# Kernel tuning notes

Hardware: AMD Instinct MI355X
Metric: run time of the kernel (lower is better)

The kernel has to match this reference:

```python
import jax, jax.numpy as jnp
import numpy as np

B, H, L, DK = 1, 16, 2048, 64
F_FACTOR = 64            # f
MAX_SEQ = 2048           # max_seq_len
RB = MAX_SEQ // F_FACTOR # 32, out dim of f_b


def setup_inputs() -> dict:
    key = jax.random.key(0)
    ks = jax.random.split(key, 6)
    q = jax.random.normal(ks[0], (B, H, L, DK), dtype=jnp.float32)
    v = jax.random.normal(ks[1], (B, H, L, DK), dtype=jnp.float32)
    # nn.Linear weights: [out_features, in_features]
    Wa = jax.random.normal(ks[2], (F_FACTOR, DK), dtype=jnp.float32) / np.sqrt(DK)
    ba = jax.random.normal(ks[3], (F_FACTOR,), dtype=jnp.float32) * 0.02
    Wb = jax.random.normal(ks[4], (RB, DK), dtype=jnp.float32) / np.sqrt(DK)
    bb = jax.random.normal(ks[5], (RB,), dtype=jnp.float32) * 0.02
    return {"q": q, "v": v, "Wa": Wa, "ba": ba, "Wb": Wb, "bb": bb, "len_q": L}


def reference(q, v, Wa, ba, Wb, bb, len_q):
    f = Wa.shape[0]            # f
    rb = Wb.shape[0]           # max_seq_len // f
    # h_a: repeat each of the f factor channels (max_seq_len//f) times -> [B,H,L,max_seq_len], slice to len_q
    h_a = jnp.repeat(q @ Wa.T + ba, rb, axis=-1)[..., :len_q]
    # h_b: repeat each of the (max_seq_len//f) channels f times
    h_b = jnp.repeat(q @ Wb.T + bb, f, axis=-1)[..., :len_q]
    # dense_attn = h_a @ h_b^T  -> [B,H,L,L]
    dense_attn = jnp.einsum('bhik,bhjk->bhij', h_a, h_b)
    # mask=None path; dropout inactive (eval / p=0)
    dense_attn = jax.nn.softmax(dense_attn, axis=-1)
    output = jnp.matmul(dense_attn, v)  # [B,H,L,DK]
    return (output, dense_attn)
```

## Files before the change

kernel.cpp:

```cpp
#include <hip/hip_runtime.h>
#include <hip/hip_bf16.h>


#define HN 16
#define LN 2048
#define KR 32

typedef __attribute__((ext_vector_type(8))) short bf16x8;
typedef __attribute__((ext_vector_type(4))) float f32x4;

__device__ __forceinline__ float b2f(unsigned short u) {
    return __uint_as_float(((unsigned int)u) << 16);
}
__device__ __forceinline__ unsigned short f2b(float f) {
    __hip_bfloat16 h = __float2bfloat16(f);
    return *reinterpret_cast<unsigned short*>(&h);
}

__global__ __launch_bounds__(256) void k_cb(
    const float* __restrict__ q,
    const float* __restrict__ Wa, const float* __restrict__ ba,
    const float* __restrict__ Wb, const float* __restrict__ bb,
    unsigned short* __restrict__ Chi, unsigned short* __restrict__ Clo,
    unsigned short* __restrict__ Bhi, unsigned short* __restrict__ Blo)
{
    __shared__ float sWa[64 * 64];
    __shared__ float sWb[32 * 64];
    __shared__ float sba[64];
    __shared__ float sbb[32];
    const int tid = threadIdx.x;
    for (int i = tid; i < 64 * 64; i += 256) sWa[i] = Wa[i];
    for (int i = tid; i < 32 * 64; i += 256) sWb[i] = Wb[i];
    if (tid < 64) sba[tid] = ba[tid];
    if (tid < 32) sbb[tid] = bb[tid];
    __syncthreads();

    const int t = blockIdx.x * 256 + tid;
    const int row = t >> 2, mh = (t & 3) * 8;
    float qf[64];
    const float4* q4p = reinterpret_cast<const float4*>(q + (size_t)row * 64);
    #pragma unroll
    for (int k4 = 0; k4 < 16; ++k4) {
        float4 u = q4p[k4];
        qf[4*k4+0] = u.x; qf[4*k4+1] = u.y; qf[4*k4+2] = u.z; qf[4*k4+3] = u.w;
    }
    const int ob = row * KR;
    #pragma unroll 1
    for (int mi = 0; mi < 8; ++mi) {
        const int m = mh + mi;
        float a0 = sba[2*m], a1 = sba[2*m+1], bv = sbb[m];
        const float4* wa0 = reinterpret_cast<const float4*>(&sWa[(2*m) * 64]);
        const float4* wa1 = reinterpret_cast<const float4*>(&sWa[(2*m+1) * 64]);
        const float4* wb0 = reinterpret_cast<const float4*>(&sWb[m * 64]);
        #pragma unroll
        for (int k4 = 0; k4 < 16; ++k4) {
            float4 w0 = wa0[k4], w1 = wa1[k4], w2 = wb0[k4];
            float x0 = qf[4*k4], x1 = qf[4*k4+1], x2 = qf[4*k4+2], x3 = qf[4*k4+3];
            a0 = fmaf(x0, w0.x, a0); a0 = fmaf(x1, w0.y, a0);
            a0 = fmaf(x2, w0.z, a0); a0 = fmaf(x3, w0.w, a0);
            a1 = fmaf(x0, w1.x, a1); a1 = fmaf(x1, w1.y, a1);
            a1 = fmaf(x2, w1.z, a1); a1 = fmaf(x3, w1.w, a1);
            bv = fmaf(x0, w2.x, bv); bv = fmaf(x1, w2.y, bv);
            bv = fmaf(x2, w2.z, bv); bv = fmaf(x3, w2.w, bv);
        }
        float c = 32.f * (a0 + a1);
        unsigned short ch = f2b(c);
        Chi[ob + m] = ch; Clo[ob + m] = f2b(c - b2f(ch));
        unsigned short bh = f2b(bv);
        Bhi[ob + m] = bh; Blo[ob + m] = f2b(bv - b2f(bh));
    }
}

__global__ __launch_bounds__(256) void k_vt(
    const float* __restrict__ v, unsigned short* __restrict__ Vt)
{
    __shared__ unsigned short sv[64 * 66];
    const int tid = threadIdx.x;
    const int h = blockIdx.x >> 5, jt = blockIdx.x & 31;
    const float* src = v + (size_t)(h * LN + jt * 64) * 64;
    for (int i = tid; i < 4096; i += 256)
        sv[(i >> 6) * 66 + (i & 63)] = f2b(src[i]);
    __syncthreads();
    for (int i = tid; i < 4096; i += 256) {
        int d = i >> 6, j = i & 63;
        Vt[(size_t)(h * 64 + d) * LN + jt * 64 + j] = sv[j * 66 + d];
    }
}

__global__ __launch_bounds__(256) void k_pvs(
    const unsigned short* __restrict__ Chi, const unsigned short* __restrict__ Clo,
    const unsigned short* __restrict__ Bhi, const unsigned short* __restrict__ Blo,
    const unsigned short* __restrict__ Vt,
    float* __restrict__ outO, float* __restrict__ outP)
{
    __shared__ unsigned short Ps[4][16 * 68];
    __shared__ float Psf[4][16 * 68];
    const int b = blockIdx.x;
    const int h = (b & 7) * 2 + (b >> 8);
    const int tile = (b >> 3) & 31;
    const int tid = threadIdx.x, w = tid >> 6, lane = tid & 63;
    const int quad = lane >> 4, n16 = lane & 15;
    const int rbase = tile * 64 + w * 16;
    const int hL = h * LN;
    unsigned short* ps = &Ps[w][0];
    float* psf = &Psf[w][0];

    const bf16x8 ahi = *reinterpret_cast<const bf16x8*>(Chi + (size_t)(hL + rbase + n16) * KR + quad * 8);
    const bf16x8 alo = *reinterpret_cast<const bf16x8*>(Clo + (size_t)(hL + rbase + n16) * KR + quad * 8);

    const unsigned short* bhiP = Bhi + (size_t)(hL + n16) * KR + quad * 8;
    const unsigned short* bloP = Blo + (size_t)(hL + n16) * KR + quad * 8;

    const unsigned short* vrow[4];
    #pragma unroll
    for (int di = 0; di < 4; ++di)
        vrow[di] = Vt + (size_t)(h * 64 + di * 16 + n16) * LN + quad * 8;

    f32x4 zero = {0.f, 0.f, 0.f, 0.f};

    float m0[4] = {-1e30f, -1e30f, -1e30f, -1e30f};
    float l0[4] = {0.f, 0.f, 0.f, 0.f};
    for (int jc = 0; jc < 32; ++jc) {
        const int jb = jc * 64;
        f32x4 s[4];
        #pragma unroll
        for (int ni = 0; ni < 4; ++ni) {
            const int off = (jb + ni * 16) * KR;
            bf16x8 bhi = *reinterpret_cast<const bf16x8*>(bhiP + off);
            bf16x8 blo = *reinterpret_cast<const bf16x8*>(bloP + off);
            f32x4 acc = zero;
            acc = __builtin_amdgcn_mfma_f32_16x16x32_bf16(ahi, bhi, acc, 0, 0, 0);
            acc = __builtin_amdgcn_mfma_f32_16x16x32_bf16(ahi, blo, acc, 0, 0, 0);
            acc = __builtin_amdgcn_mfma_f32_16x16x32_bf16(alo, bhi, acc, 0, 0, 0);
            acc = __builtin_amdgcn_mfma_f32_16x16x32_bf16(alo, blo, acc, 0, 0, 0);
            s[ni] = acc;
        }
        #pragma unroll
        for (int r = 0; r < 4; ++r) {
            float v0 = s[0][r], v1 = s[1][r], v2 = s[2][r], v3 = s[3][r];
            float mx = fmaxf(fmaxf(v0, v1), fmaxf(v2, v3));
            float mn = fmaxf(m0[r], mx);
            l0[r] = l0[r] * __expf(m0[r] - mn)
                  + __expf(v0 - mn) + __expf(v1 - mn)
                  + __expf(v2 - mn) + __expf(v3 - mn);
            m0[r] = mn;
        }
    }
    #pragma unroll
    for (int off = 1; off <= 8; off <<= 1) {
        #pragma unroll
        for (int r = 0; r < 4; ++r) {
            float m2 = __shfl_xor(m0[r], off, 64);
            float l2 = __shfl_xor(l0[r], off, 64);
            float mn = fmaxf(m0[r], m2);
            l0[r] = l0[r] * __expf(m0[r] - mn) + l2 * __expf(m2 - mn);
            m0[r] = mn;
        }
    }
    float mr[4], li[4];
    #pragma unroll
    for (int r = 0; r < 4; ++r) { mr[r] = m0[r]; li[r] = 1.f / l0[r]; }

    f32x4 o[4];
    #pragma unroll
    for (int di = 0; di < 4; ++di) o[di] = zero;

    for (int jc = 0; jc < 32; ++jc) {
        const int jb = jc * 64;
        #pragma unroll
        for (int ni = 0; ni < 4; ++ni) {
            const int off = (jb + ni * 16) * KR;
            bf16x8 bhi = *reinterpret_cast<const bf16x8*>(bhiP + off);
            bf16x8 blo = *reinterpret_cast<const bf16x8*>(bloP + off);
            f32x4 acc = zero;
            acc = __builtin_amdgcn_mfma_f32_16x16x32_bf16(ahi, bhi, acc, 0, 0, 0);
            acc = __builtin_amdgcn_mfma_f32_16x16x32_bf16(ahi, blo, acc, 0, 0, 0);
            acc = __builtin_amdgcn_mfma_f32_16x16x32_bf16(alo, bhi, acc, 0, 0, 0);
            acc = __builtin_amdgcn_mfma_f32_16x16x32_bf16(alo, blo, acc, 0, 0, 0);
            #pragma unroll
            for (int r = 0; r < 4; ++r) {
                float p = __expf(acc[r] - mr[r]) * li[r];
                const int sidx = (quad * 4 + r) * 68 + ni * 16 + n16;
                psf[sidx] = p;
                ps[sidx] = f2b(p);
            }
        }
        #pragma unroll
        for (int rr = 0; rr < 4; ++rr) {
            const int prow = rr * 4 + quad;
            const int pcol = n16 * 4;
            f32x4 val = *reinterpret_cast<f32x4*>(psf + prow * 68 + pcol);
            __builtin_nontemporal_store(val,
                reinterpret_cast<f32x4*>(outP + (size_t)(hL + rbase + prow) * LN + jb + pcol));
        }
        #pragma unroll
        for (int ks = 0; ks < 2; ++ks) {
            const bf16x8 pa = *reinterpret_cast<const bf16x8*>(ps + n16 * 68 + ks * 32 + quad * 8);
            #pragma unroll
            for (int di = 0; di < 4; ++di) {
                const bf16x8 vb = *reinterpret_cast<const bf16x8*>(vrow[di] + jb + ks * 32);
                o[di] = __builtin_amdgcn_mfma_f32_16x16x32_bf16(pa, vb, o[di], 0, 0, 0);
            }
        }
    }
    #pragma unroll
    for (int di = 0; di < 4; ++di) {
        #pragma unroll
        for (int r = 0; r < 4; ++r) {
            const int grow = rbase + quad * 4 + r;
            __builtin_nontemporal_store(o[di][r],
                &outO[(size_t)(hL + grow) * 64 + di * 16 + n16]);
        }
    }
}

extern "C" void kernel_launch(void* const* d_in, const int* in_sizes, int n_in,
                              void* d_out, int out_size, void* d_ws, size_t ws_size,
                              hipStream_t stream)
{
    (void)in_sizes; (void)n_in; (void)out_size; (void)ws_size;
    const float* q  = (const float*)d_in[0];
    const float* v  = (const float*)d_in[1];
    const float* Wa = (const float*)d_in[2];
    const float* ba = (const float*)d_in[3];
    const float* Wb = (const float*)d_in[4];
    const float* bb = (const float*)d_in[5];

    float* out = (float*)d_out;
    char* wsb = (char*)d_ws;
    const size_t CBb = (size_t)HN * LN * KR * 2;
    unsigned short* Chi = (unsigned short*)(wsb + 0 * CBb);
    unsigned short* Clo = (unsigned short*)(wsb + 1 * CBb);
    unsigned short* Bhi = (unsigned short*)(wsb + 2 * CBb);
    unsigned short* Blo = (unsigned short*)(wsb + 3 * CBb);
    unsigned short* Vt  = (unsigned short*)(wsb + 4 * CBb);

    float* outO = out;
    float* outP = out + (size_t)HN * LN * 64;

    hipLaunchKernelGGL(k_cb, dim3(512), dim3(256), 0, stream,
                       q, Wa, ba, Wb, bb, Chi, Clo, Bhi, Blo);
    hipLaunchKernelGGL(k_vt, dim3(512), dim3(256), 0, stream, v, Vt);
    hipLaunchKernelGGL(k_pvs, dim3(512), dim3(256), 0, stream,
                       Chi, Clo, Bhi, Blo, Vt, outO, outP);
}
```

Measured before the change: 449.6 us.

## Pack B and V into per-chunk fragment tiles staged via direct global-to-LDS loads

The B hi/lo factors and transposed V are now written into a combined per-head, per-64-column tile whose layout matches the MFMA fragment order. The attention kernel stages each tile into shared memory with global_load_lds and reads its fragments from LDS instead of issuing scattered global loads per wave. The producer kernels gain vectorized 16-byte stores. The cost is two block barriers per chunk iteration and extra LDS, with no double buffering, so load latency is no longer hidden by per-wave independence.

```diff
diff --git a/kernel.cpp b/kernel.cpp
--- a/kernel.cpp
+++ b/kernel.cpp
@@ -16,13 +16,20 @@
     __hip_bfloat16 h = __float2bfloat16(f);
     return *reinterpret_cast<unsigned short*>(&h);
 }
+__device__ __forceinline__ void glds16(const void* g, void* l) {
+    __builtin_amdgcn_global_load_lds(
+        (const __attribute__((address_space(1))) unsigned int*)g,
+        (__attribute__((address_space(3))) unsigned int*)l, 16, 0, 0);
+}
+
+#define TILE_SH 8192
 
 __global__ __launch_bounds__(256) void k_cb(
     const float* __restrict__ q,
     const float* __restrict__ Wa, const float* __restrict__ ba,
     const float* __restrict__ Wb, const float* __restrict__ bb,
     unsigned short* __restrict__ Chi, unsigned short* __restrict__ Clo,
-    unsigned short* __restrict__ Bhi, unsigned short* __restrict__ Blo)
+    unsigned short* __restrict__ Tile)
 {
     __shared__ float sWa[64 * 64];
     __shared__ float sWb[32 * 64];
@@ -36,7 +43,10 @@
     __syncthreads();
 
     const int t = blockIdx.x * 256 + tid;
-    const int row = t >> 2, mh = (t & 3) * 8;
+    const int row = t >> 2, kg = t & 3, mh = kg * 8;
+    const int h = row >> 11, i = row & 2047;
+    const int jc = i >> 6, c = i & 63;
+
     float qf[64];
     const float4* q4p = reinterpret_cast<const float4*>(q + (size_t)row * 64);
     #pragma unroll
@@ -44,8 +54,8 @@
         float4 u = q4p[k4];
         qf[4*k4+0] = u.x; qf[4*k4+1] = u.y; qf[4*k4+2] = u.z; qf[4*k4+3] = u.w;
     }
-    const int ob = row * KR;
-    #pragma unroll 1
+    unsigned short chb[8], clb[8], bhb[8], blb[8];
+    #pragma unroll
     for (int mi = 0; mi < 8; ++mi) {
         const int m = mh + mi;
         float a0 = sba[2*m], a1 = sba[2*m+1], bv = sbb[m];
@@ -63,36 +73,48 @@
             bv = fmaf(x0, w2.x, bv); bv = fmaf(x1, w2.y, bv);
             bv = fmaf(x2, w2.z, bv); bv = fmaf(x3, w2.w, bv);
         }
-        float c = 32.f * (a0 + a1);
-        unsigned short ch = f2b(c);
-        Chi[ob + m] = ch; Clo[ob + m] = f2b(c - b2f(ch));
+        float cc = 32.f * (a0 + a1);
+        unsigned short ch = f2b(cc);
+        chb[mi] = ch; clb[mi] = f2b(cc - b2f(ch));
         unsigned short bh = f2b(bv);
-        Bhi[ob + m] = bh; Blo[ob + m] = f2b(bv - b2f(bh));
-    }
-}
-
-__global__ __launch_bounds__(256) void k_vt(
-    const float* __restrict__ v, unsigned short* __restrict__ Vt)
+        bhb[mi] = bh; blb[mi] = f2b(bv - b2f(bh));
+    }
+    *reinterpret_cast<uint4*>(Chi + (size_t)row * KR + mh) = *reinterpret_cast<uint4*>(chb);
+    *reinterpret_cast<uint4*>(Clo + (size_t)row * KR + mh) = *reinterpret_cast<uint4*>(clb);
+    unsigned short* tb = Tile + (size_t)(h * 32 + jc) * TILE_SH + (kg * 64 + c) * 8;
+    *reinterpret_cast<uint4*>(tb)        = *reinterpret_cast<uint4*>(bhb);
+    *reinterpret_cast<uint4*>(tb + 2048) = *reinterpret_cast<uint4*>(blb);
+}
+
+__global__ __launch_bounds__(256) void k_vtc(
+    const float* __restrict__ v, unsigned short* __restrict__ Tile)
 {
     __shared__ unsigned short sv[64 * 66];
     const int tid = threadIdx.x;
-    const int h = blockIdx.x >> 5, jt = blockIdx.x & 31;
-    const float* src = v + (size_t)(h * LN + jt * 64) * 64;
+    const int h = blockIdx.x >> 5, jc = blockIdx.x & 31;
+    const float* src = v + (size_t)(h * LN + jc * 64) * 64;
     for (int i = tid; i < 4096; i += 256)
         sv[(i >> 6) * 66 + (i & 63)] = f2b(src[i]);
     __syncthreads();
-    for (int i = tid; i < 4096; i += 256) {
-        int d = i >> 6, j = i & 63;
-        Vt[(size_t)(h * 64 + d) * LN + jt * 64 + j] = sv[j * 66 + d];
+    unsigned short* vt = Tile + (size_t)(h * 32 + jc) * TILE_SH + 4096;
+    #pragma unroll
+    for (int it = 0; it < 2; ++it) {
+        const int gi = tid + it * 256;
+        const int jg = gi >> 6, d = gi & 63;
+        unsigned short g8[8];
+        #pragma unroll
+        for (int cjj = 0; cjj < 8; ++cjj)
+            g8[cjj] = sv[(jg * 8 + cjj) * 66 + d];
+        *reinterpret_cast<uint4*>(vt + (jg * 64 + d) * 8) = *reinterpret_cast<uint4*>(g8);
     }
 }
 
 __global__ __launch_bounds__(256) void k_pvs(
     const unsigned short* __restrict__ Chi, const unsigned short* __restrict__ Clo,
-    const unsigned short* __restrict__ Bhi, const unsigned short* __restrict__ Blo,
-    const unsigned short* __restrict__ Vt,
+    const unsigned short* __restrict__ Tile,
     float* __restrict__ outO, float* __restrict__ outP)
 {
+    __shared__ unsigned short sT[TILE_SH];
     __shared__ unsigned short Ps[4][16 * 68];
     __shared__ float Psf[4][16 * 68];
     const int b = blockIdx.x;
@@ -108,26 +130,25 @@
     const bf16x8 ahi = *reinterpret_cast<const bf16x8*>(Chi + (size_t)(hL + rbase + n16) * KR + quad * 8);
     const bf16x8 alo = *reinterpret_cast<const bf16x8*>(Clo + (size_t)(hL + rbase + n16) * KR + quad * 8);
 
-    const unsigned short* bhiP = Bhi + (size_t)(hL + n16) * KR + quad * 8;
-    const unsigned short* bloP = Blo + (size_t)(hL + n16) * KR + quad * 8;
-
-    const unsigned short* vrow[4];
-    #pragma unroll
-    for (int di = 0; di < 4; ++di)
-        vrow[di] = Vt + (size_t)(h * 64 + di * 16 + n16) * LN + quad * 8;
+    const char* tBase = (const char*)(Tile + (size_t)(h * 32) * TILE_SH);
+    char* sTb = (char*)sT;
+    const int fragB = (quad * 64 + n16) * 8;
+    const int lane16 = lane * 16;
 
     f32x4 zero = {0.f, 0.f, 0.f, 0.f};
 
     float m0[4] = {-1e30f, -1e30f, -1e30f, -1e30f};
     float l0[4] = {0.f, 0.f, 0.f, 0.f};
     for (int jc = 0; jc < 32; ++jc) {
-        const int jb = jc * 64;
+        const char* g = tBase + (size_t)jc * (TILE_SH * 2);
+        glds16(g + w * 1024 + lane16,      sTb + w * 1024);
+        glds16(g + (w + 4) * 1024 + lane16, sTb + (w + 4) * 1024);
+        __syncthreads();
         f32x4 s[4];
         #pragma unroll
         for (int ni = 0; ni < 4; ++ni) {
-            const int off = (jb + ni * 16) * KR;
-            bf16x8 bhi = *reinterpret_cast<const bf16x8*>(bhiP + off);
-            bf16x8 blo = *reinterpret_cast<const bf16x8*>(bloP + off);
+            bf16x8 bhi = *reinterpret_cast<const bf16x8*>(sT + fragB + ni * 128);
+            bf16x8 blo = *reinterpret_cast<const bf16x8*>(sT + 2048 + fragB + ni * 128);
             f32x4 acc = zero;
             acc = __builtin_amdgcn_mfma_f32_16x16x32_bf16(ahi, bhi, acc, 0, 0, 0);
             acc = __builtin_amdgcn_mfma_f32_16x16x32_bf16(ahi, blo, acc, 0, 0, 0);
@@ -145,6 +166,7 @@
                   + __expf(v2 - mn) + __expf(v3 - mn);
             m0[r] = mn;
         }
+        __syncthreads();
     }
     #pragma unroll
     for (int off = 1; off <= 8; off <<= 1) {
@@ -167,11 +189,16 @@
 
     for (int jc = 0; jc < 32; ++jc) {
         const int jb = jc * 64;
+        const char* g = tBase + (size_t)jc * (TILE_SH * 2);
+        glds16(g + w * 1024 + lane16,        sTb + w * 1024);
+        glds16(g + (w + 4) * 1024 + lane16,  sTb + (w + 4) * 1024);
+        glds16(g + (w + 8) * 1024 + lane16,  sTb + (w + 8) * 1024);
+        glds16(g + (w + 12) * 1024 + lane16, sTb + (w + 12) * 1024);
+        __syncthreads();
         #pragma unroll
         for (int ni = 0; ni < 4; ++ni) {
-            const int off = (jb + ni * 16) * KR;
-            bf16x8 bhi = *reinterpret_cast<const bf16x8*>(bhiP + off);
-            bf16x8 blo = *reinterpret_cast<const bf16x8*>(bloP + off);
+            bf16x8 bhi = *reinterpret_cast<const bf16x8*>(sT + fragB + ni * 128);
+            bf16x8 blo = *reinterpret_cast<const bf16x8*>(sT + 2048 + fragB + ni * 128);
             f32x4 acc = zero;
             acc = __builtin_amdgcn_mfma_f32_16x16x32_bf16(ahi, bhi, acc, 0, 0, 0);
             acc = __builtin_amdgcn_mfma_f32_16x16x32_bf16(ahi, blo, acc, 0, 0, 0);
@@ -198,10 +225,12 @@
             const bf16x8 pa = *reinterpret_cast<const bf16x8*>(ps + n16 * 68 + ks * 32 + quad * 8);
             #pragma unroll
             for (int di = 0; di < 4; ++di) {
-                const bf16x8 vb = *reinterpret_cast<const bf16x8*>(vrow[di] + jb + ks * 32);
+                const bf16x8 vb = *reinterpret_cast<const bf16x8*>(
+                    sT + 4096 + ((ks * 4 + quad) * 64 + di * 16 + n16) * 8);
                 o[di] = __builtin_amdgcn_mfma_f32_16x16x32_bf16(pa, vb, o[di], 0, 0, 0);
             }
         }
+        __syncthreads();
     }
     #pragma unroll
     for (int di = 0; di < 4; ++di) {
@@ -229,18 +258,16 @@
     float* out = (float*)d_out;
     char* wsb = (char*)d_ws;
     const size_t CBb = (size_t)HN * LN * KR * 2;
-    unsigned short* Chi = (unsigned short*)(wsb + 0 * CBb);
-    unsigned short* Clo = (unsigned short*)(wsb + 1 * CBb);
-    unsigned short* Bhi = (unsigned short*)(wsb + 2 * CBb);
-    unsigned short* Blo = (unsigned short*)(wsb + 3 * CBb);
-    unsigned short* Vt  = (unsigned short*)(wsb + 4 * CBb);
+    unsigned short* Chi  = (unsigned short*)(wsb + 0 * CBb);
+    unsigned short* Clo  = (unsigned short*)(wsb + 1 * CBb);
+    unsigned short* Tile = (unsigned short*)(wsb + 2 * CBb);
 
     float* outO = out;
     float* outP = out + (size_t)HN * LN * 64;
 
     hipLaunchKernelGGL(k_cb, dim3(512), dim3(256), 0, stream,
-                       q, Wa, ba, Wb, bb, Chi, Clo, Bhi, Blo);
-    hipLaunchKernelGGL(k_vt, dim3(512), dim3(256), 0, stream, v, Vt);
+                       q, Wa, ba, Wb, bb, Chi, Clo, Tile);
+    hipLaunchKernelGGL(k_vtc, dim3(512), dim3(256), 0, stream, v, Tile);
     hipLaunchKernelGGL(k_pvs, dim3(512), dim3(256), 0, stream,
-                       Chi, Clo, Bhi, Blo, Vt, outO, outP);
-}
+                       Chi, Clo, Tile, outO, outP);
+}
```

Measured after the change: 389.4 us. -13.4%, faster.
